# Kernel tuning notes

Hardware: AMD Instinct MI355X
Metric: run time of the kernel (lower is better)

Reference implementation:

```python
import jax, jax.numpy as jnp
import numpy as np

HIDDEN = 128
LOCAL_HEADS = 4
GLOBAL_HEADS = 2
N_NODES = 10000
E_LOCAL = 320000
E_GLOBAL = 640000
NEG_SLOPE = 0.2  # PyG GATv2Conv default


def _glorot(key, shape):
    fan_in, fan_out = shape[0], shape[-1]
    s = jnp.sqrt(6.0 / (fan_in + fan_out))
    return jax.random.uniform(key, shape, jnp.float32, -s, s)


def setup_inputs() -> dict:
    key = jax.random.key(0)
    ks = jax.random.split(key, 16)
    H1, H2 = LOCAL_HEADS, GLOBAL_HEADS
    d = HIDDEN
    inp = {
        "x": jax.random.normal(ks[0], (N_NODES, d), jnp.float32),
        "edge_index": jax.random.randint(ks[1], (2, E_LOCAL), 0, N_NODES, jnp.int32),
        "global_edge_index": jax.random.randint(ks[2], (2, E_GLOBAL), 0, N_NODES, jnp.int32),
        # conv1 (local) params
        "Wl1": _glorot(ks[3], (d, H1 * d)),
        "bl1": jnp.zeros((H1 * d,), jnp.float32),
        "Wr1": _glorot(ks[4], (d, H1 * d)),
        "br1": jnp.zeros((H1 * d,), jnp.float32),
        "att1": _glorot(ks[5], (H1, d)),
        "b1": jnp.zeros((H1 * d,), jnp.float32),
        # conv2 (global) params
        "Wl2": _glorot(ks[6], (d, H2 * d)),
        "bl2": jnp.zeros((H2 * d,), jnp.float32),
        "Wr2": _glorot(ks[7], (d, H2 * d)),
        "br2": jnp.zeros((H2 * d,), jnp.float32),
        "att2": _glorot(ks[8], (H2, d)),
        "b2": jnp.zeros((H2 * d,), jnp.float32),
        # final fc: hidden*(H1+H2) -> hidden
        "Wfc": _glorot(ks[9], (d * (H1 + H2), d)),
        "bfc": jnp.zeros((d,), jnp.float32),
    }
    return inp


def gatv2_layer(x, edge, Wl, bl, Wr, br, att, bias, heads):
    # PyG GATv2Conv: concat=True, add_self_loops=True, share_weights=False
    N = x.shape[0]
    HC = Wl.shape[1]
    C = HC // heads
    loops = jnp.arange(N, dtype=edge.dtype)
    src = jnp.concatenate([edge[0], loops])  # message source j
    dst = jnp.concatenate([edge[1], loops])  # message target i
    xl = (x @ Wl + bl).reshape(N, heads, C)  # source transform
    xr = (x @ Wr + br).reshape(N, heads, C)  # target transform
    s = jax.nn.leaky_relu(xl[src] + xr[dst], NEG_SLOPE)        # [E,H,C]
    logits = jnp.einsum('ehc,hc->eh', s, att)                   # [E,H]
    m = jax.ops.segment_max(logits, dst, num_segments=N)       # segment softmax
    a = jnp.exp(logits - m[dst])
    denom = jax.ops.segment_sum(a, dst, num_segments=N)
    alpha = a / denom[dst]                                      # [E,H]
    out = jax.ops.segment_sum(alpha[:, :, None] * xl[src], dst, num_segments=N)
    return out.reshape(N, HC) + bias


def reference(x, edge_index, global_edge_index,
              Wl1, bl1, Wr1, br1, att1, b1,
              Wl2, bl2, Wr2, br2, att2, b2,
              Wfc, bfc):
    x1 = gatv2_layer(x, edge_index, Wl1, bl1, Wr1, br1, att1, b1, LOCAL_HEADS)
    x2 = gatv2_layer(x, global_edge_index, Wl2, bl2, Wr2, br2, att2, b2, GLOBAL_HEADS)
    h = jnp.concatenate([x1, x2], axis=-1)  # [N, hidden*(H1+H2)]
    return h @ Wfc + bfc                     # [N, hidden]
```

## Files before the change

### kernel.cpp

```cpp
#include <hip/hip_runtime.h>

#define N_NODES 10000
#define E_LOCAL 320000
#define E_GLOBAL 640000
#define CNT_LEN 10240
#define NB 160
#define BCAP1 3072
#define BCAP2 5632
#define CHUNK 2048
#define NWG_L 157
#define NWG_G 313

typedef __attribute__((ext_vector_type(8))) short short8;
typedef __attribute__((ext_vector_type(4))) float f32x4;
typedef __attribute__((ext_vector_type(4))) unsigned short ushort4v;
typedef __attribute__((ext_vector_type(2))) unsigned int uint2v;
typedef __attribute__((ext_vector_type(4))) unsigned int uint4v;

typedef __attribute__((address_space(1))) const void* gas_ptr;
typedef __attribute__((address_space(3))) void* lds_ptr;

__device__ __forceinline__ unsigned short f2bf(float f) {
  union { unsigned int i; float f; } v; v.f = f;
  unsigned int r = (v.i + 0x7FFF + ((v.i >> 16) & 1)) >> 16;
  return (unsigned short)r;
}
__device__ __forceinline__ void gld_lds16(const void* g, void* l) {
  __builtin_amdgcn_global_load_lds((gas_ptr)g, (lds_ptr)l, 16, 0, 0);
}

template<int NW> struct WVecT;
template<> struct WVecT<4> { using T = uint4v; };
template<> struct WVecT<2> { using T = uint2v; };

template<int NW, typename WV>
__device__ __forceinline__ void w2f(WV w, float* f) {
  #pragma unroll
  for (int i = 0; i < NW; ++i) {
    union { unsigned int u; float x; } lo, hi;
    lo.u = w[i] << 16; hi.u = w[i] & 0xffff0000u;
    f[2 * i] = lo.x; f[2 * i + 1] = hi.x;
  }
}

template<int CTRL>
__device__ __forceinline__ float dppadd(float v) {
  int s = __builtin_amdgcn_update_dpp(0, __float_as_int(v), CTRL, 0xf, 0xf, true);
  return v + __int_as_float(s);
}
__device__ __forceinline__ float red16(float v) {
  v = dppadd<0xB1>(v);
  v = dppadd<0x4E>(v);
  v = dppadd<0x140>(v);
  v = dppadd<0x141>(v);
  return v;
}

__global__ __launch_bounds__(256) void prep(
    const float* __restrict__ x,
    const float* __restrict__ Wl1, const float* __restrict__ Wr1,
    const float* __restrict__ Wl2, const float* __restrict__ Wr2,
    const float* __restrict__ Wfc,
    const float* __restrict__ bl1, const float* __restrict__ br1,
    const float* __restrict__ bl2, const float* __restrict__ br2,
    ushort* __restrict__ xb, ushort* __restrict__ wt_all,
    ushort* __restrict__ wtfc, float* __restrict__ bias_all,
    int* __restrict__ bcur) {
  __shared__ float tl[32][33];
  int b = blockIdx.x;
  const int tid = threadIdx.x;
  if (b < 1250) {
    int i = b * 256 + tid;
    if (i < 320000) {
      float4 f = reinterpret_cast<const float4*>(x)[i];
      ushort4v o; o[0] = f2bf(f.x); o[1] = f2bf(f.y); o[2] = f2bf(f.z); o[3] = f2bf(f.w);
      reinterpret_cast<ushort4v*>(xb)[i] = o;
    }
    return;
  }
  b -= 1250;
  if (b < 288) {
    const float* W; ushort* dst; int N, nOff, ldK; int t = b;
    if (t < 64)       { W = Wl1; dst = wt_all; N = 512; nOff = 0;    ldK = 128; }
    else if (t < 128) { W = Wr1; dst = wt_all; N = 512; nOff = 512;  ldK = 128; t -= 64; }
    else if (t < 160) { W = Wl2; dst = wt_all; N = 256; nOff = 1024; ldK = 128; t -= 128; }
    else if (t < 192) { W = Wr2; dst = wt_all; N = 256; nOff = 1280; ldK = 128; t -= 160; }
    else              { W = Wfc; dst = wtfc;   N = 128; nOff = 0;    ldK = 768; t -= 192; }
    const int ntn = N / 32;
    const int n0 = (t % ntn) * 32, k0 = (t / ntn) * 32;
    const int tx = tid & 31, ty = tid >> 5;
    #pragma unroll
    for (int j = 0; j < 4; ++j)
      tl[ty + j * 8][tx] = W[(size_t)(k0 + ty + j * 8) * N + n0 + tx];
    __syncthreads();
    #pragma unroll
    for (int j = 0; j < 4; ++j)
      dst[(size_t)(nOff + n0 + ty + j * 8) * ldK + k0 + tx] = f2bf(tl[tx][ty + j * 8]);
    return;
  }
  for (int i = tid; i < 1536; i += 256) {
    float v = i < 512 ? bl1[i] : i < 1024 ? br1[i - 512]
            : i < 1280 ? bl2[i - 1024] : br2[i - 1280];
    bias_all[i] = v;
  }
  for (int i = tid; i < 2 * NB; i += 256) bcur[i] = 0;
}

template<bool OUT_BF16, int K>
__global__ __launch_bounds__(256) void gemm_mfma(
    const ushort* __restrict__ A,
    const ushort* __restrict__ Bt,
    const float* __restrict__ bias,
    void* __restrict__ outv, int M, int N, int ldOut) {
  __shared__ ushort As[2][64 * 32];
  __shared__ ushort Bs[2][64 * 32];
  const int tid  = threadIdx.x;
  const int wave = tid >> 6;
  const int lane = tid & 63;
  const int row0 = blockIdx.y * 64;
  const int col0 = blockIdx.x * 64;
  const int srow = tid >> 2;
  const int schunk = tid & 3;
  int ar = row0 + srow; if (ar >= M) ar = M - 1;
  const ushort* aSrc = A  + (size_t)ar * K + schunk * 8;
  const ushort* bSrc = Bt + (size_t)(col0 + srow) * K + schunk * 8;
  const int ldsOff = tid * 8;
  const int fr = lane & 15;
  const int kc = lane >> 4;

  f32x4 c[4];
  #pragma unroll
  for (int f = 0; f < 4; ++f) { c[f][0] = 0.f; c[f][1] = 0.f; c[f][2] = 0.f; c[f][3] = 0.f; }

  constexpr int NK = K / 32;
  gld_lds16(aSrc, &As[0][ldsOff]);
  gld_lds16(bSrc, &Bs[0][ldsOff]);
  #pragma unroll
  for (int kk = 0; kk < NK; ++kk) {
    const int cur = kk & 1;
    __syncthreads();
    if (kk + 1 < NK) {
      gld_lds16(aSrc + (kk + 1) * 32, &As[cur ^ 1][ldsOff]);
      gld_lds16(bSrc + (kk + 1) * 32, &Bs[cur ^ 1][ldsOff]);
    }
    short8 a = *reinterpret_cast<const short8*>(&As[cur][(wave * 16 + fr) * 32 + kc * 8]);
    #pragma unroll
    for (int f = 0; f < 4; ++f) {
      short8 b = *reinterpret_cast<const short8*>(&Bs[cur][(f * 16 + fr) * 32 + kc * 8]);
      c[f] = __builtin_amdgcn_mfma_f32_16x16x32_bf16(a, b, c[f], 0, 0, 0);
    }
  }
  const int orow = row0 + wave * 16 + (lane >> 4) * 4;
  #pragma unroll
  for (int f = 0; f < 4; ++f) {
    const int col = col0 + f * 16 + fr;
    const float bv = bias ? bias[col] : 0.f;
    #pragma unroll
    for (int q = 0; q < 4; ++q) {
      const int r = orow + q;
      if (r < M) {
        float v = c[f][q] + bv;
        if (OUT_BF16) ((ushort*)outv)[(size_t)r * ldOut + col] = f2bf(v);
        else          ((float*) outv)[(size_t)r * ldOut + col] = v;
      }
    }
  }
}

__global__ __launch_bounds__(256) void bucketize(
    const int* __restrict__ sl, const int* __restrict__ dl,
    const int* __restrict__ sg, const int* __restrict__ dg,
    int* __restrict__ bcur, uint2* __restrict__ bb1, uint2* __restrict__ bb2) {
  __shared__ int h[NB];
  __shared__ int cur[NB];
  const int tid = threadIdx.x;
  int wg = blockIdx.x;
  const int* S; const int* D; int E0, Etot; uint2* BB; int* BC; int cap;
  if (wg < NWG_L) { S = sl; D = dl; E0 = wg * CHUNK; Etot = E_LOCAL;  BB = bb1; BC = bcur;      cap = BCAP1; }
  else { wg -= NWG_L; S = sg; D = dg; E0 = wg * CHUNK; Etot = E_GLOBAL; BB = bb2; BC = bcur + NB; cap = BCAP2; }
  for (int i = tid; i < NB; i += 256) h[i] = 0;
  __syncthreads();
  int myd[8], mys[8];
  #pragma unroll
  for (int k = 0; k < 8; ++k) {
    int e = E0 + k * 256 + tid;
    if (e < Etot) { myd[k] = D[e]; mys[k] = S[e]; atomicAdd(&h[myd[k] >> 6], 1); }
    else myd[k] = -1;
  }
  __syncthreads();
  for (int b = tid; b < NB; b += 256)
    cur[b] = h[b] ? atomicAdd(&BC[b], h[b]) : 0;
  __syncthreads();
  #pragma unroll
  for (int k = 0; k < 8; ++k) {
    if (myd[k] >= 0) {
      int b = myd[k] >> 6;
      int pos = atomicAdd(&cur[b], 1);
      if (pos < cap) BB[(size_t)b * cap + pos] = make_uint2((unsigned)mys[k], (unsigned)myd[k]);
    }
  }
}

__global__ __launch_bounds__(320) void scanb(const int* __restrict__ bcur,
                                             int* __restrict__ base) {
  __shared__ int v[2 * NB];
  __shared__ int sz[2 * NB];
  const int t = threadIdx.x;
  const int ls = (t < NB) ? 0 : NB;
  int s = min(bcur[t], (t < NB) ? BCAP1 : BCAP2);
  sz[t] = s; v[t] = s;
  __syncthreads();
  for (int o = 1; o < NB; o <<= 1) {
    int add = (t - o >= ls) ? v[t - o] : 0;
    __syncthreads();
    v[t] += add;
    __syncthreads();
  }
  base[t] = v[t] - sz[t];
}

__global__ __launch_bounds__(256) void csrbuild(
    const int* __restrict__ bcur, const int* __restrict__ base,
    const uint2* __restrict__ bb1, const uint2* __restrict__ bb2,
    int* __restrict__ csr1, int* __restrict__ csr2,
    int* __restrict__ off1, int* __restrict__ off2) {
  __shared__ int nh[64];
  __shared__ int ncur[64];
  const int tid = threadIdx.x;
  const int b = blockIdx.x;
  const uint2* BB; int* csr; int* off; int cap; int bi;
  if (b < NB) { BB = bb1; csr = csr1; off = off1; cap = BCAP1; bi = b; }
  else        { BB = bb2; csr = csr2; off = off2; cap = BCAP2; bi = b - NB; }
  const int n = min(bcur[b], cap);
  const uint2* P = BB + (size_t)bi * cap;
  if (tid < 64) nh[tid] = 0;
  __syncthreads();
  for (int i = tid; i < n; i += 256) atomicAdd(&nh[P[i].y & 63], 1);
  __syncthreads();
  if (tid == 0) {
    int s = base[b];
    #pragma unroll 4
    for (int j = 0; j < 64; ++j) { int c = nh[j]; nh[j] = s; s += c; }
  }
  __syncthreads();
  if (tid < 64) { off[bi * 64 + tid] = nh[tid]; ncur[tid] = nh[tid]; }
  __syncthreads();
  for (int i = tid; i < n; i += 256) {
    uint2 p = P[i];
    int pos = atomicAdd(&ncur[p.y & 63], 1);
    csr[pos] = (int)p.x;
  }
}

template<int H, int U>
__global__ __launch_bounds__(256) void aggregate(
    const ushort* __restrict__ xl, const ushort* __restrict__ xr,
    const float* __restrict__ att, const int* __restrict__ csr,
    const int* __restrict__ off, const float* __restrict__ bias,
    int inLd, ushort* __restrict__ outp, int outLd) {
  constexpr int TC = H * 128;
  constexpr int PER = TC / 64;
  constexpr int NW = PER / 2;
  constexpr int GRP = 64 / H;
  using WVec = typename WVecT<NW>::T;
  const int lane = threadIdx.x & 63;
  const int node = (int)(((long)blockIdx.x * blockDim.x + threadIdx.x) >> 6);
  if (node >= N_NODES) return;
  const int base = lane * PER;

  float attv[PER], xri[PER], acc[PER];
  #pragma unroll
  for (int p = 0; p < PER; ++p) attv[p] = att[base + p];
  {
    WVec r = *reinterpret_cast<const WVec*>(&xr[(size_t)node * inLd + base]);
    w2f<NW>(r, xri);
  }

  float den;
  {
    WVec r = *reinterpret_cast<const WVec*>(&xl[(size_t)node * inLd + base]);
    float xs[PER]; w2f<NW>(r, xs);
    float part = 0.f;
    #pragma unroll
    for (int p = 0; p < PER; ++p) {
      float t = xs[p] + xri[p];
      t = fmaxf(t, 0.2f * t);
      part = fmaf(t, attv[p], part);
    }
    part = red16(part);
    if (GRP == 32) part += __shfl_xor(part, 16, 64);
    den = __expf(part);
    #pragma unroll
    for (int p = 0; p < PER; ++p) acc[p] = den * xs[p];
  }

  const int e0 = off[node];
  const int e1 = off[node + 1];
  const int nfull = (e1 - e0) / U;
  WVec rA[U], rB[U];
  int iC[U], iN[U];
  if (nfull > 0) {
    #pragma unroll
    for (int m = 0; m < U; ++m) iC[m] = csr[e0 + m];
    #pragma unroll
    for (int m = 0; m < U; ++m)
      rA[m] = *reinterpret_cast<const WVec*>(&xl[(size_t)iC[m] * inLd + base]);
    if (nfull > 1) {
      #pragma unroll
      for (int m = 0; m < U; ++m) iC[m] = csr[e0 + U + m];
    }
  }
  for (int b = 0; b < nfull; ++b) {
    if (b + 2 < nfull) {
      #pragma unroll
      for (int m = 0; m < U; ++m) iN[m] = csr[e0 + (b + 2) * U + m];
    }
    if (b + 1 < nfull) {
      #pragma unroll
      for (int m = 0; m < U; ++m)
        rB[m] = *reinterpret_cast<const WVec*>(&xl[(size_t)iC[m] * inLd + base]);
    }
    float pp[U];
    #pragma unroll
    for (int m = 0; m < U; ++m) {
      float xs[PER]; w2f<NW>(rA[m], xs);
      float d = 0.f;
      #pragma unroll
      for (int p = 0; p < PER; ++p) {
        float t = xs[p] + xri[p];
        t = fmaxf(t, 0.2f * t);
        d = fmaf(t, attv[p], d);
      }
      pp[m] = d;
    }
    #pragma unroll
    for (int m = 0; m < U; ++m) pp[m] = red16(pp[m]);
    if (GRP == 32) {
      #pragma unroll
      for (int m = 0; m < U; ++m) pp[m] += __shfl_xor(pp[m], 16, 64);
    }
    #pragma unroll
    for (int m = 0; m < U; ++m) {
      float w = __expf(pp[m]);
      den += w;
      float xs[PER]; w2f<NW>(rA[m], xs);
      #pragma unroll
      for (int p = 0; p < PER; ++p) acc[p] = fmaf(w, xs[p], acc[p]);
    }
    #pragma unroll
    for (int m = 0; m < U; ++m) { rA[m] = rB[m]; iC[m] = iN[m]; }
  }
  for (int e = e0 + nfull * U; e < e1; ++e) {
    int s = csr[e];
    WVec r = *reinterpret_cast<const WVec*>(&xl[(size_t)s * inLd + base]);
    float xs[PER]; w2f<NW>(r, xs);
    float d = 0.f;
    #pragma unroll
    for (int p = 0; p < PER; ++p) {
      float t = xs[p] + xri[p];
      t = fmaxf(t, 0.2f * t);
      d = fmaf(t, attv[p], d);
    }
    d = red16(d);
    if (GRP == 32) d += __shfl_xor(d, 16, 64);
    float w = __expf(d);
    den += w;
    #pragma unroll
    for (int p = 0; p < PER; ++p) acc[p] = fmaf(w, xs[p], acc[p]);
  }

  const float inv = 1.f / den;
  #pragma unroll
  for (int v = 0; v < PER / 4; ++v) {
    ushort4v o;
    #pragma unroll
    for (int q = 0; q < 4; ++q)
      o[q] = f2bf(fmaf(acc[v * 4 + q], inv, bias[base + v * 4 + q]));
    *reinterpret_cast<ushort4v*>(&outp[(size_t)node * outLd + base + v * 4]) = o;
  }
}

extern "C" void kernel_launch(void* const* d_in, const int* in_sizes, int n_in,
                              void* d_out, int out_size, void* d_ws, size_t ws_size,
                              hipStream_t stream) {
  const float* x    = (const float*)d_in[0];
  const int*   ei   = (const int*)d_in[1];
  const int*   gei  = (const int*)d_in[2];
  const float* Wl1  = (const float*)d_in[3];
  const float* bl1  = (const float*)d_in[4];
  const float* Wr1  = (const float*)d_in[5];
  const float* br1  = (const float*)d_in[6];
  const float* att1 = (const float*)d_in[7];
  const float* b1   = (const float*)d_in[8];
  const float* Wl2  = (const float*)d_in[9];
  const float* bl2  = (const float*)d_in[10];
  const float* Wr2  = (const float*)d_in[11];
  const float* br2  = (const float*)d_in[12];
  const float* att2 = (const float*)d_in[13];
  const float* b2   = (const float*)d_in[14];
  const float* Wfc  = (const float*)d_in[15];
  const float* bfc  = (const float*)d_in[16];
  float* out = (float*)d_out;

  char* w = (char*)d_ws;
  ushort* xb     = (ushort*)w; w += (size_t)N_NODES * 128 * 2;
  ushort* feat   = (ushort*)w; w += (size_t)N_NODES * 1536 * 2;
  ushort* hb     = (ushort*)w; w += (size_t)N_NODES * 768 * 2;
  ushort* wt_all = (ushort*)w; w += (size_t)1536 * 128 * 2;
  ushort* wtfc   = (ushort*)w; w += (size_t)128 * 768 * 2;
  float* bias_all = (float*)w; w += 1536 * 4;
  int* off1 = (int*)w;            w += (size_t)CNT_LEN * 4;
  int* off2 = (int*)w;            w += (size_t)CNT_LEN * 4;
  int* csr1 = (int*)w;            w += (size_t)E_LOCAL * 4;
  int* csr2 = (int*)w;            w += (size_t)E_GLOBAL * 4;
  int* bcur = (int*)w;            w += 2 * NB * 4;
  int* bbase = (int*)w;           w += 2 * NB * 4;
  uint2* bb1 = (uint2*)w;         w += (size_t)NB * BCAP1 * 8;
  uint2* bb2 = (uint2*)w;         w += (size_t)NB * BCAP2 * 8;

  const int N = N_NODES;
  prep<<<1539, 256, 0, stream>>>(x, Wl1, Wr1, Wl2, Wr2, Wfc,
                                 bl1, br1, bl2, br2,
                                 xb, wt_all, wtfc, bias_all, bcur);

  bucketize<<<NWG_L + NWG_G, 256, 0, stream>>>(
      ei, ei + E_LOCAL, gei, gei + E_GLOBAL, bcur, bb1, bb2);
  scanb<<<1, 320, 0, stream>>>(bcur, bbase);
  csrbuild<<<2 * NB, 256, 0, stream>>>(bcur, bbase, bb1, bb2,
                                       csr1, csr2, off1, off2);

  gemm_mfma<true, 128><<<dim3(24, 157), 256, 0, stream>>>(
      xb, wt_all, bias_all, feat, N, 1536, 1536);

  aggregate<4, 3><<<(N * 64 + 255) / 256, 256, 0, stream>>>(
      feat, feat + 512, att1, csr1, off1, b1, 1536, hb, 768);
  aggregate<2, 4><<<(N * 64 + 255) / 256, 256, 0, stream>>>(
      feat + 1024, feat + 1280, att2, csr2, off2, b2, 1536, hb + 512, 768);

  gemm_mfma<false, 768><<<dim3(2, 157), 256, 0, stream>>>(hb, wtfc, bfc, out, N, 128, 128);
}
```

Baseline: 246.9 us.

## Split each node's edge aggregation across four waves and fuse both GAT layers

Aggregation now assigns one 256-thread block per node and splits that node's edge range across four waves. Partial weighted sums and denominators are combined through shared memory. The local and global layers run in a single launch, blockIdx selecting which layer a block handles. The attention vector is prescaled by log2(e) so exp2f replaces __expf, and the software prefetch is restructured into a ping-pong double buffer. The aim is more memory-level parallelism per node and less launch overhead, at the cost of a block-wide sync plus LDS reduction per node and fewer edges per wave.

```diff
diff --git a/kernel.cpp b/kernel.cpp
--- a/kernel.cpp
+++ b/kernel.cpp
@@ -108,10 +108,9 @@
 
 template<bool OUT_BF16, int K>
 __global__ __launch_bounds__(256) void gemm_mfma(
-    const ushort* __restrict__ A,
-    const ushort* __restrict__ Bt,
-    const float* __restrict__ bias,
-    void* __restrict__ outv, int M, int N, int ldOut) {
+    const ushort* __restrict__ A, const ushort* __restrict__ Bt,
+    const float* __restrict__ bias, void* __restrict__ outv,
+    int M, int N, int ldOut) {
   __shared__ ushort As[2][64 * 32];
   __shared__ ushort Bs[2][64 * 32];
   const int tid  = threadIdx.x;
@@ -253,81 +252,75 @@
 }
 
 template<int H, int U>
-__global__ __launch_bounds__(256) void aggregate(
+__device__ __forceinline__ void agg_block(
     const ushort* __restrict__ xl, const ushort* __restrict__ xr,
     const float* __restrict__ att, const int* __restrict__ csr,
     const int* __restrict__ off, const float* __restrict__ bias,
-    int inLd, ushort* __restrict__ outp, int outLd) {
+    int inLd, ushort* __restrict__ outp, int outLd, int node,
+    float* __restrict__ sacc, float* __restrict__ sden) {
   constexpr int TC = H * 128;
   constexpr int PER = TC / 64;
   constexpr int NW = PER / 2;
   constexpr int GRP = 64 / H;
   using WVec = typename WVecT<NW>::T;
-  const int lane = threadIdx.x & 63;
-  const int node = (int)(((long)blockIdx.x * blockDim.x + threadIdx.x) >> 6);
-  if (node >= N_NODES) return;
+  const int tid = threadIdx.x;
+  const int wave = tid >> 6;
+  const int lane = tid & 63;
   const int base = lane * PER;
+  const int head = lane / GRP;
 
   float attv[PER], xri[PER], acc[PER];
   #pragma unroll
-  for (int p = 0; p < PER; ++p) attv[p] = att[base + p];
+  for (int p = 0; p < PER; ++p) attv[p] = att[base + p] * 1.4426950408889634f;
   {
     WVec r = *reinterpret_cast<const WVec*>(&xr[(size_t)node * inLd + base]);
     w2f<NW>(r, xri);
   }
-
-  float den;
-  {
+  #pragma unroll
+  for (int p = 0; p < PER; ++p) acc[p] = 0.f;
+  float den = 0.f;
+
+  const int e0n = off[node], e1n = off[node + 1];
+  const int chunk = (e1n - e0n + 3) >> 2;
+  const int e0 = e0n + wave * chunk;
+  const int e1 = min(e0 + chunk, e1n);
+
+  if (wave == 0) {
     WVec r = *reinterpret_cast<const WVec*>(&xl[(size_t)node * inLd + base]);
     float xs[PER]; w2f<NW>(r, xs);
-    float part = 0.f;
+    float d = 0.f;
     #pragma unroll
     for (int p = 0; p < PER; ++p) {
       float t = xs[p] + xri[p];
       t = fmaxf(t, 0.2f * t);
-      part = fmaf(t, attv[p], part);
-    }
-    part = red16(part);
-    if (GRP == 32) part += __shfl_xor(part, 16, 64);
-    den = __expf(part);
-    #pragma unroll
-    for (int p = 0; p < PER; ++p) acc[p] = den * xs[p];
-  }
-
-  const int e0 = off[node];
-  const int e1 = off[node + 1];
-  const int nfull = (e1 - e0) / U;
-  WVec rA[U], rB[U];
-  int iC[U], iN[U];
-  if (nfull > 0) {
-    #pragma unroll
-    for (int m = 0; m < U; ++m) iC[m] = csr[e0 + m];
+      d = fmaf(t, attv[p], d);
+    }
+    d = red16(d);
+    if (GRP == 32) d += __shfl_xor(d, 16, 64);
+    float wgt = exp2f(d);
+    den = wgt;
+    #pragma unroll
+    for (int p = 0; p < PER; ++p) acc[p] = wgt * xs[p];
+  }
+
+  auto loadIdx = [&](int bb, int* ii) {
+    #pragma unroll
+    for (int m = 0; m < U; ++m) ii[m] = csr[e0 + bb * U + m];
+  };
+  auto loadRows = [&](const int* ii, WVec* rr) {
     #pragma unroll
     for (int m = 0; m < U; ++m)
-      rA[m] = *reinterpret_cast<const WVec*>(&xl[(size_t)iC[m] * inLd + base]);
-    if (nfull > 1) {
-      #pragma unroll
-      for (int m = 0; m < U; ++m) iC[m] = csr[e0 + U + m];
-    }
-  }
-  for (int b = 0; b < nfull; ++b) {
-    if (b + 2 < nfull) {
-      #pragma unroll
-      for (int m = 0; m < U; ++m) iN[m] = csr[e0 + (b + 2) * U + m];
-    }
-    if (b + 1 < nfull) {
-      #pragma unroll
-      for (int m = 0; m < U; ++m)
-        rB[m] = *reinterpret_cast<const WVec*>(&xl[(size_t)iC[m] * inLd + base]);
-    }
-    float pp[U];
+      rr[m] = *reinterpret_cast<const WVec*>(&xl[(size_t)ii[m] * inLd + base]);
+  };
+  auto computeB = [&](WVec* rr) {
+    float pp[U]; float xs[U][PER];
     #pragma unroll
     for (int m = 0; m < U; ++m) {
-      float xs[PER]; w2f<NW>(rA[m], xs);
+      w2f<NW>(rr[m], xs[m]);
       float d = 0.f;
       #pragma unroll
       for (int p = 0; p < PER; ++p) {
-        float t = xs[p] + xri[p];
+        float t = xs[m][p] + xri[p];
         t = fmaxf(t, 0.2f * t);
         d = fmaf(t, attv[p], d);
       }
@@ -341,16 +334,29 @@
     }
     #pragma unroll
     for (int m = 0; m < U; ++m) {
-      float w = __expf(pp[m]);
-      den += w;
-      float xs[PER]; w2f<NW>(rA[m], xs);
+      float wgt = exp2f(pp[m]);
+      den += wgt;
       #pragma unroll
-      for (int p = 0; p < PER; ++p) acc[p] = fmaf(w, xs[p], acc[p]);
-    }
-    #pragma unroll
-    for (int m = 0; m < U; ++m) { rA[m] = rB[m]; iC[m] = iN[m]; }
-  }
-  for (int e = e0 + nfull * U; e < e1; ++e) {
+      for (int p = 0; p < PER; ++p) acc[p] = fmaf(wgt, xs[m][p], acc[p]);
+    }
+  };
+
+  const int nb = (e1 - e0) / U;
+  WVec rA[U], rB[U];
+  int iA[U], iB[U];
+  if (nb > 0) { loadIdx(0, iA); loadRows(iA, rA); }
+  if (nb > 1) loadIdx(1, iB);
+  int b = 0;
+  for (; b + 2 <= nb; b += 2) {
+    loadRows(iB, rB);
+    if (b + 2 < nb) loadIdx(b + 2, iA);
+    computeB(rA);
+    if (b + 2 < nb) loadRows(iA, rA);
+    if (b + 3 < nb) loadIdx(b + 3, iB);
+    computeB(rB);
+  }
+  if (b < nb) computeB(rA);
+  for (int e = e0 + nb * U; e < e1; ++e) {
     int s = csr[e];
     WVec r = *reinterpret_cast<const WVec*>(&xl[(size_t)s * inLd + base]);
     float xs[PER]; w2f<NW>(r, xs);
@@ -363,21 +369,44 @@
     }
     d = red16(d);
     if (GRP == 32) d += __shfl_xor(d, 16, 64);
-    float w = __expf(d);
-    den += w;
-    #pragma unroll
-    for (int p = 0; p < PER; ++p) acc[p] = fmaf(w, xs[p], acc[p]);
-  }
-
-  const float inv = 1.f / den;
-  #pragma unroll
-  for (int v = 0; v < PER / 4; ++v) {
-    ushort4v o;
-    #pragma unroll
-    for (int q = 0; q < 4; ++q)
-      o[q] = f2bf(fmaf(acc[v * 4 + q], inv, bias[base + v * 4 + q]));
-    *reinterpret_cast<ushort4v*>(&outp[(size_t)node * outLd + base + v * 4]) = o;
-  }
+    float wgt = exp2f(d);
+    den += wgt;
+    #pragma unroll
+    for (int p = 0; p < PER; ++p) acc[p] = fmaf(wgt, xs[p], acc[p]);
+  }
+
+  #pragma unroll
+  for (int p = 0; p < PER; ++p) sacc[wave * TC + base + p] = acc[p];
+  if ((lane & (GRP - 1)) == 0) sden[wave * H + head] = den;
+  __syncthreads();
+  constexpr int CH = TC / 256;
+  #pragma unroll
+  for (int j = 0; j < CH; ++j) {
+    const int c = tid * CH + j;
+    float s = sacc[c] + sacc[TC + c] + sacc[2 * TC + c] + sacc[3 * TC + c];
+    const int h = c >> 7;
+    float dt = sden[h] + sden[H + h] + sden[2 * H + h] + sden[3 * H + h];
+    outp[(size_t)node * outLd + c] = f2bf(s / dt + bias[c]);
+  }
+}
+
+__global__ __launch_bounds__(256) void aggregate2(
+    const ushort* __restrict__ feat,
+    const float* __restrict__ att1, const float* __restrict__ att2,
+    const int* __restrict__ csr1, const int* __restrict__ off1,
+    const float* __restrict__ b1,
+    const int* __restrict__ csr2, const int* __restrict__ off2,
+    const float* __restrict__ b2,
+    ushort* __restrict__ hb) {
+  __shared__ float sacc[4 * 512];
+  __shared__ float sden[16];
+  const int nd = blockIdx.x;
+  if (nd < N_NODES)
+    agg_block<4, 3>(feat, feat + 512, att1, csr1, off1, b1, 1536, hb, 768,
+                    nd, sacc, sden);
+  else
+    agg_block<2, 4>(feat + 1024, feat + 1280, att2, csr2, off2, b2, 1536,
+                    hb + 512, 768, nd - N_NODES, sacc, sden);
 }
 
 extern "C" void kernel_launch(void* const* d_in, const int* in_sizes, int n_in,
@@ -432,10 +461,8 @@
   gemm_mfma<true, 128><<<dim3(24, 157), 256, 0, stream>>>(
       xb, wt_all, bias_all, feat, N, 1536, 1536);
 
-  aggregate<4, 3><<<(N * 64 + 255) / 256, 256, 0, stream>>>(
-      feat, feat + 512, att1, csr1, off1, b1, 1536, hb, 768);
-  aggregate<2, 4><<<(N * 64 + 255) / 256, 256, 0, stream>>>(
-      feat + 1024, feat + 1280, att2, csr2, off2, b2, 1536, hb + 512, 768);
+  aggregate2<<<2 * N, 256, 0, stream>>>(feat, att1, att2,
+                                        csr1, off1, b1, csr2, off2, b2, hb);
 
   gemm_mfma<false, 768><<<dim3(2, 157), 256, 0, stream>>>(hb, wtfc, bfc, out, N, 128, 128);
 }
```

New measurement: 254.5 us. 1.03x slower.
